# Optimization experiments

Hardware: AMD Instinct MI355X
Metric: run time of the kernel (lower is better)

Reference implementation:

```python
import jax, jax.numpy as jnp
import numpy as np

F, H1, H2, K, L = 16, 64, 64, 8, 8          # n_features, hidden sizes, num_bins, num_layers
NBP = 3 * K + 1                              # num_bijector_params per feature
RMIN, RMAX = -10.0, 10.0
MIN_BIN, MIN_SLOPE = 1e-4, 1e-4              # distrax RationalQuadraticSpline defaults


def setup_inputs() -> dict:
    key = jax.random.key(0)
    ks = jax.random.split(key, 11)
    B = 131072
    return {
        "x": jax.random.normal(ks[0], (B, F), jnp.float32),
        "W0": jax.random.normal(ks[1], (L, F, F), jnp.float32) * 0.1,
        "b0": jax.random.normal(ks[2], (L, F), jnp.float32) * 0.01,
        "W1": jax.random.normal(ks[3], (L, F, H1), jnp.float32) * 0.1,
        "b1": jax.random.normal(ks[4], (L, H1), jnp.float32) * 0.01,
        "W2": jax.random.normal(ks[5], (L, H1, H2), jnp.float32) * 0.1,
        "b2": jax.random.normal(ks[6], (L, H2), jnp.float32) * 0.01,
        "Wout": jax.random.normal(ks[7], (L, H2, F * NBP), jnp.float32) * 0.05,
        "bout": jax.random.normal(ks[8], (L, F * NBP), jnp.float32) * 0.01,
        # scalar-affine coupling params; scale kept positive (init is ones in the module)
        "scale": jnp.exp(0.05 * jax.random.normal(ks[9], (L, F), jnp.float32)),
        "shift": jax.random.normal(ks[10], (L, F), jnp.float32) * 0.1,
    }


def _rq_spline_fwd(params, x):
    """distrax.RationalQuadraticSpline forward_and_log_det (elementwise).
    params: (B, F, 3K+1), x: (B, F) -> (y, log_det) each (B, F)."""
    uw, uh, ud = params[..., :K], params[..., K:2 * K], params[..., 2 * K:]
    total = RMAX - RMIN
    w = jax.nn.softmax(uw, axis=-1) * (total - K * MIN_BIN) + MIN_BIN   # bin widths
    h = jax.nn.softmax(uh, axis=-1) * (total - K * MIN_BIN) + MIN_BIN   # bin heights
    offset = float(np.log(np.expm1(1.0 - MIN_SLOPE)))                   # softplus(0+offset)=1
    d = jax.nn.softplus(ud + offset) + MIN_SLOPE                        # knot slopes (B,F,K+1)
    zeros = jnp.zeros(w.shape[:-1] + (1,), w.dtype)
    xpos = RMIN + jnp.concatenate([zeros, jnp.cumsum(w, -1)], -1)       # knot x (B,F,K+1)
    ypos = RMIN + jnp.concatenate([zeros, jnp.cumsum(h, -1)], -1)       # knot y (B,F,K+1)
    # per-element bin search
    idx = jnp.clip(jnp.sum((x[..., None] >= xpos).astype(jnp.int32), -1) - 1, 0, K - 1)
    take = lambda a: jnp.take_along_axis(a, idx[..., None], axis=-1)[..., 0]
    xk, xk1 = take(xpos[..., :-1]), take(xpos[..., 1:])
    yk, yk1 = take(ypos[..., :-1]), take(ypos[..., 1:])
    dk, dk1 = take(d[..., :-1]), take(d[..., 1:])
    bw = xk1 - xk
    bh = yk1 - yk
    s = bh / bw                                                          # bin slope
    z = jnp.clip((x - xk) / bw, 0.0, 1.0)
    z1m = 1.0 - z
    den = s + (dk1 + dk - 2.0 * s) * z * z1m
    y = yk + bh * (s * z * z + dk * z * z1m) / den
    num_ld = dk1 * z * z + 2.0 * s * z * z1m + dk * z1m * z1m
    ld = 2.0 * jnp.log(s) + jnp.log(num_ld) - 2.0 * jnp.log(den)
    outside = (x <= RMIN) | (x >= RMAX)                                  # identity outside range
    return jnp.where(outside, x, y), jnp.where(outside, 0.0, ld)


def reference(x, W0, b0, W1, b1, W2, b2, Wout, bout, scale, shift):
    """log_prob of Transformed(base, Inverse(Chain(layers))) == base.log_prob(Chain.fwd(x)) + fwd logdet."""
    B = x.shape[0]
    feat = jnp.arange(F)
    z = x
    logdet = jnp.zeros((B,), x.dtype)
    # distrax.Chain applies the last-appended layer first -> iterate layers in reverse;
    # within layer i: spline coupling (appended second) then scalar-affine coupling.
    for i in reversed(range(L)):
        mask = ((feat + i) % 2).astype(bool)        # True = pass-through / conditioner input
        mz = jnp.where(mask, z, 0.0)
        hid = jnp.tanh(mz @ W0[i] + b0[i])
        hid = jnp.tanh(hid @ W1[i] + b1[i])
        hid = hid @ W2[i] + b2[i]                   # last MLP layer is linear
        p = (hid @ Wout[i] + bout[i]).reshape(B, F, NBP)
        y, ld = _rq_spline_fwd(p, z)
        z = jnp.where(mask, z, y)
        logdet = logdet + jnp.sum(jnp.where(mask, 0.0, ld), axis=-1)
        # scalar affine coupling with all-False mask: transforms every feature
        z = z * scale[i] + shift[i]
        logdet = logdet + jnp.sum(jnp.log(jnp.abs(scale[i])))
    base_lp = -0.5 * jnp.sum(z * z, axis=-1) - 0.5 * F * float(np.log(2.0 * np.pi))
    return base_lp + logdet
```

## Files before the change

### kernel.cpp

```cpp
#include <hip/hip_runtime.h>
#include <math.h>

typedef _Float16 f16;
typedef _Float16 half4 __attribute__((ext_vector_type(4)));
typedef _Float16 half8 __attribute__((ext_vector_type(8)));
typedef float f32x4  __attribute__((ext_vector_type(4)));
typedef float f32x16 __attribute__((ext_vector_type(16)));

#define DEV __device__ __forceinline__

#define W1F_OFF 0
#define W2F_OFF 16384
#define WOF_OFF 81920
#define B1T_OFF 344064
#define B2T_OFF 346112
#define SUMLOG_OFF 352256
#define W0F_OFF 352320
#define B0T_OFF 361088
#define BOT_OFF 363136

#define H0_OFF    0
#define H0_STRIDE 48
#define H_OFF     3072
#define H_STRIDE  152
#define P_OFF     0
#define P_STRIDE  112
#define ARENA     12800
#define LDS_BYTES (4 * ARENA)

DEV float frcp(float x){ return __builtin_amdgcn_rcpf(x); }

#if __has_builtin(__builtin_amdgcn_exp2f)
DEV float fexp2(float x){ return __builtin_amdgcn_exp2f(x); }
#else
DEV float fexp2(float x){ return exp2f(x); }
#endif
#if __has_builtin(__builtin_amdgcn_logf)
DEV float flog2(float x){ return __builtin_amdgcn_logf(x); }
#else
DEV float flog2(float x){ return log2f(x); }
#endif

#define LN2F    0.69314718056f
#define LOG2EF  1.4426950409f
#define TWOLOG2EF 2.8853900818f

DEV float ftanh2(float x){
  float e = fexp2(x);
  float r = frcp(e + 1.f);
  return fmaf(-2.f, r, 1.f);
}

DEV void rq_spline(const float p[25], float xv, float &y_out, float &ld_out)
{
  float ew[8]; float sw = 0.f;
#pragma unroll
  for (int k = 0; k < 8; ++k){ ew[k] = fexp2(p[k]); sw += ew[k]; }
  float rw = frcp(sw) * 19.9992f;

  float xpos[9];
  xpos[0] = -10.f;
#pragma unroll
  for (int k = 0; k < 8; ++k) xpos[k + 1] = xpos[k] + fmaf(ew[k], rw, 1e-4f);

  bool b[8];
  int idx = 0;
#pragma unroll
  for (int j = 1; j < 8; ++j){ b[j] = (xv >= xpos[j]); idx += b[j] ? 1 : 0; }

  float xk = xpos[0], ewk = ew[0];
#pragma unroll
  for (int j = 1; j < 8; ++j){
    xk  = b[j] ? xpos[j] : xk;
    ewk = b[j] ? ew[j]   : ewk;
  }
  float bw = fmaf(ewk, rw, 1e-4f);

  float eh[8]; float shs = 0.f;
#pragma unroll
  for (int k = 0; k < 8; ++k){ eh[k] = fexp2(p[8 + k]); shs += eh[k]; }
  float rh = frcp(shs) * 19.9992f;

  float S = 0.f, ehk = eh[0];
#pragma unroll
  for (int k = 1; k < 8; ++k){
    S   += b[k] ? eh[k - 1] : 0.f;
    ehk  = b[k] ? eh[k]     : ehk;
  }
  float yk = fmaf(S, rh, fmaf((float)idx, 1e-4f, -10.f));
  float bh = fmaf(ehk, rh, 1e-4f);

  float vA = p[16], vB = p[17];
#pragma unroll
  for (int j = 1; j < 8; ++j){
    vA = b[j] ? p[16 + j] : vA;
    vB = b[j] ? p[17 + j] : vB;
  }
  float tA = fmaxf(vA, 0.f) + flog2(1.f + fexp2(-fabsf(vA)));
  float dk  = fmaf(LN2F, tA, 1e-4f);
  float tB = fmaxf(vB, 0.f) + flog2(1.f + fexp2(-fabsf(vB)));
  float dk1 = fmaf(LN2F, tB, 1e-4f);

  float rbw = frcp(bw);
  float s   = bh * rbw;
  float zf  = fminf(fmaxf((xv - xk) * rbw, 0.f), 1.f);
  float z1  = 1.f - zf;
  float zz  = zf * zf, z01 = zf * z1;
  float den = s + (dk1 + dk - 2.f * s) * z01;
  float rden = frcp(den);
  float yv  = yk + bh * (s * zz + dk * z01) * rden;
  float num = dk1 * zz + 2.f * s * z01 + dk * z1 * z1;
  float ldv2 = flog2(s * s * num * rden * rden);

  bool outside = (xv <= -10.f) || (xv >= 10.f);
  y_out  = outside ? xv : yv;
  ld_out = outside ? 0.f : ldv2;
}

extern "C" __global__ void __launch_bounds__(256)
prep_kernel(const float* __restrict__ W0, const float* __restrict__ b0,
            const float* __restrict__ W1, const float* __restrict__ b1,
            const float* __restrict__ W2, const float* __restrict__ b2,
            const float* __restrict__ Wo, const float* __restrict__ bout,
            const float* __restrict__ scale, char* __restrict__ ws)
{
  int tid = blockIdx.x * 256 + threadIdx.x;
  if (tid < 1024){
    int fi = tid >> 6, lane = tid & 63;
    int l = fi >> 1, nt = fi & 1;
    int n = nt * 32 + (lane & 31), khi = lane >> 5;
    half8 h;
#pragma unroll
    for (int j = 0; j < 8; ++j){ int k = khi * 8 + j; h[j] = (f16)(W1[l * 1024 + k * 64 + n] * TWOLOG2EF); }
    *(half8*)(ws + W1F_OFF + fi * 1024 + lane * 16) = h;
  } else if (tid < 5120){
    int idx = tid - 1024;
    int fi = idx >> 6, lane = idx & 63;
    int l = fi >> 3, kt = (fi >> 1) & 3, nt = fi & 1;
    int n = nt * 32 + (lane & 31), khi = lane >> 5;
    half8 h;
#pragma unroll
    for (int j = 0; j < 8; ++j){ int k = kt * 16 + khi * 8 + j; h[j] = (f16)W2[l * 4096 + k * 64 + n]; }
    *(half8*)(ws + W2F_OFF + fi * 1024 + lane * 16) = h;
  } else if (tid < 21504){
    int idx = tid - 5120;
    int fi = idx >> 6, lane = idx & 63;
    int l = fi >> 5, u = (fi >> 2) & 7, kt = fi & 3;
    int f = (l & 1) + 2 * u;
    int c = lane & 31, khi = lane >> 5;
    half8 h;
#pragma unroll
    for (int j = 0; j < 8; ++j){
      int k = kt * 16 + khi * 8 + j;
      float v = (c < 25) ? Wo[l * 25600 + k * 400 + f * 25 + c] * LOG2EF : 0.f;
      h[j] = (f16)v;
    }
    *(half8*)(ws + WOF_OFF + fi * 1024 + lane * 16) = h;
  } else if (tid < 22016){
    int idx = tid - 21504;
    int l = idx >> 6, nt = (idx >> 5) & 1, kh = (idx >> 4) & 1, i = idx & 15;
    int r = (i & 3) + 8 * (i >> 2) + 4 * kh;
    ((float*)(ws + B1T_OFF))[idx] = b1[l * 64 + nt * 32 + r] * TWOLOG2EF;
  } else if (tid < 22528){
    int idx = tid - 22016;
    int l = idx >> 6, nt = (idx >> 5) & 1, kh = (idx >> 4) & 1, i = idx & 15;
    int r = (i & 3) + 8 * (i >> 2) + 4 * kh;
    ((float*)(ws + B2T_OFF))[idx] = b2[l * 64 + nt * 32 + r];
  } else if (tid == 23552){
    float acc = 0.f;
    for (int i = 0; i < 128; ++i) acc += logf(fabsf(scale[i]));
    *(float*)(ws + SUMLOG_OFF) = acc;
  } else if (tid > 23552 && tid < 24065){
    int idx = tid - 23553;
    int l = idx >> 6, lane = idx & 63;
    int n = lane & 31, kh5 = lane >> 5;
    half8 h;
#pragma unroll
    for (int j = 0; j < 8; ++j){
      int k = kh5 * 8 + j;
      float v = 0.f;
      if (n < 16 && (((k + l) & 1) == 1))
        v = W0[l * 256 + k * 16 + n] * TWOLOG2EF;
      h[j] = (f16)v;
    }
    *(half8*)(ws + W0F_OFF + idx * 16) = h;
  } else if (tid >= 24065 && tid < 24321){
    int idx = tid - 24065;
    int l = idx >> 5, kh = (idx >> 4) & 1, i = idx & 15;
    int r = (i & 3) + 8 * (i >> 2) + 4 * kh;
    float v = (r < 16) ? b0[l * 16 + r] * TWOLOG2EF : 0.f;
    ((float*)(ws + B0T_OFF))[idx] = v;
  } else if (tid >= 26241 && tid < 28289){
    int idx = tid - 26241;
    int l = idx >> 8, u = (idx >> 5) & 7, kh = (idx >> 4) & 1, i = idx & 15;
    int f = (l & 1) + 2 * u;
    int r = (i & 3) + 8 * (i >> 2) + 4 * kh;
    float v = 0.f;
    if (r < 25){
      v = bout[l * 400 + f * 25 + r];
      if (r >= 16) v += 0.54116666f;
      v *= LOG2EF;
    }
    ((float*)(ws + BOT_OFF))[idx] = v;
  }
}

DEV void load_botv(const char* __restrict__ ws, int l, int u, int khi,
                   float (&botv)[16])
{
  const f32x4* bp = (const f32x4*)(ws + BOT_OFF) + ((l * 8 + u) * 2 + khi) * 4;
  f32x4 q0 = bp[0], q1 = bp[1], q2 = bp[2], q3 = bp[3];
#pragma unroll
  for (int i = 0; i < 4; ++i){
    botv[i] = q0[i]; botv[4 + i] = q1[i]; botv[8 + i] = q2[i]; botv[12 + i] = q3[i];
  }
}

DEV half8 ld_h8_pair(const char* p)
{
  half4 lo = *(const half4*)(p);
  half4 hi = *(const half4*)(p + 8);
  half8 r;
#pragma unroll
  for (int i = 0; i < 4; ++i){ r[i] = lo[i]; r[4 + i] = hi[i]; }
  return r;
}

DEV void wout_feature(const half8 (&a2)[2][4], const half8 (&bfn)[4],
                      const float (&botv)[16], char* ldsw, int ln31, int khi)
{
  f32x16 dp[2];
#pragma unroll
  for (int mt = 0; mt < 2; ++mt)
#pragma unroll
    for (int i = 0; i < 16; ++i) dp[mt][i] = botv[i];
#pragma unroll
  for (int kt = 0; kt < 4; ++kt)
#pragma unroll
    for (int mt = 0; mt < 2; ++mt)
      dp[mt] = __builtin_amdgcn_mfma_f32_32x32x16_f16(bfn[kt], a2[mt][kt], dp[mt], 0, 0, 0);
#pragma unroll
  for (int mt = 0; mt < 2; ++mt){
    int s = mt * 32 + ln31;
    char* base = ldsw + P_OFF + s * P_STRIDE + khi * 16;
    f32x4 c0, c1, c2;
#pragma unroll
    for (int i = 0; i < 4; ++i){
      c0[i] = dp[mt][i];
      c1[i] = dp[mt][4 + i];
      c2[i] = dp[mt][8 + i];
    }
    *(f32x4*)(base)      = c0;
    *(f32x4*)(base + 32) = c1;
    *(f32x4*)(base + 64) = c2;
    if (khi == 0)
      *(float*)(base + 96) = dp[mt][12];
  }
}

template<int PAR>
DEV void layer_mfma(int l,
                    const float* __restrict__ scv, const float* __restrict__ shv,
                    const char* __restrict__ ws, char* ldsw,
                    float (&z)[16], float &logdet,
                    int lane, int ln31, int khi)
{
  const half8* W1F = (const half8*)(ws + W1F_OFF);
  const half8* W2F = (const half8*)(ws + W2F_OFF);
  half8 w0f = *(const half8*)(ws + W0F_OFF + (l * 64 + lane) * 16);
  half8 w1f[2];
#pragma unroll
  for (int nt = 0; nt < 2; ++nt) w1f[nt] = W1F[(l * 2 + nt) * 64 + lane];
  half8 w2f[8];
#pragma unroll
  for (int kt = 0; kt < 4; ++kt)
#pragma unroll
    for (int nt = 0; nt < 2; ++nt)
      w2f[kt * 2 + nt] = W2F[((l * 4 + kt) * 2 + nt) * 64 + lane];

  {
    half8 zlo, zhi;
#pragma unroll
    for (int j = 0; j < 8; ++j){ zlo[j] = (f16)z[j]; zhi[j] = (f16)z[8 + j]; }
    *(half8*)(ldsw + H0_OFF + lane * H0_STRIDE)      = zlo;
    *(half8*)(ldsw + H0_OFF + lane * H0_STRIDE + 16) = zhi;
  }
  f32x16 d0t[2];
  {
    const f32x4* bp = (const f32x4*)(ws + B0T_OFF) + (l * 2 + khi) * 4;
    f32x4 q0 = bp[0], q1 = bp[1], q2 = bp[2], q3 = bp[3];
#pragma unroll
    for (int mt = 0; mt < 2; ++mt)
#pragma unroll
      for (int i = 0; i < 4; ++i){
        d0t[mt][i] = q0[i]; d0t[mt][4 + i] = q1[i];
        d0t[mt][8 + i] = q2[i]; d0t[mt][12 + i] = q3[i];
      }
  }
  {
    half8 zf[2];
#pragma unroll
    for (int mt = 0; mt < 2; ++mt)
      zf[mt] = *(const half8*)(ldsw + H0_OFF + (mt * 32 + ln31) * H0_STRIDE + khi * 16);
#pragma unroll
    for (int mt = 0; mt < 2; ++mt)
      d0t[mt] = __builtin_amdgcn_mfma_f32_32x32x16_f16(w0f, zf[mt], d0t[mt], 0, 0, 0);
  }
#pragma unroll
  for (int mt = 0; mt < 2; ++mt){
    int s = mt * 32 + ln31;
#pragma unroll
    for (int g = 0; g < 2; ++g){
      half4 h4;
#pragma unroll
      for (int j = 0; j < 4; ++j) h4[j] = (f16)ftanh2(d0t[mt][g * 4 + j]);
      *(half4*)(ldsw + H0_OFF + s * H0_STRIDE + g * 16 + khi * 8) = h4;
    }
  }

  half8 a0[2];
#pragma unroll
  for (int mt = 0; mt < 2; ++mt)
    a0[mt] = *(const half8*)(ldsw + H0_OFF + (mt * 32 + ln31) * H0_STRIDE + khi * 16);
  f32x16 d1t[2][2];
  {
    const f32x4* B1T = (const f32x4*)(ws + B1T_OFF);
#pragma unroll
    for (int nt = 0; nt < 2; ++nt){
      const f32x4* bp = B1T + ((l * 2 + nt) * 2 + khi) * 4;
      f32x4 q0 = bp[0], q1 = bp[1], q2 = bp[2], q3 = bp[3];
#pragma unroll
      for (int mt = 0; mt < 2; ++mt)
#pragma unroll
        for (int i = 0; i < 4; ++i){
          d1t[nt][mt][i] = q0[i]; d1t[nt][mt][4 + i] = q1[i];
          d1t[nt][mt][8 + i] = q2[i]; d1t[nt][mt][12 + i] = q3[i];
        }
    }
  }
#pragma unroll
  for (int nt = 0; nt < 2; ++nt)
#pragma unroll
    for (int mt = 0; mt < 2; ++mt)
      d1t[nt][mt] = __builtin_amdgcn_mfma_f32_32x32x16_f16(w1f[nt], a0[mt], d1t[nt][mt], 0, 0, 0);
#pragma unroll
  for (int nt = 0; nt < 2; ++nt)
#pragma unroll
    for (int mt = 0; mt < 2; ++mt){
      int s = mt * 32 + ln31;
#pragma unroll
      for (int g = 0; g < 4; ++g){
        half4 h4;
#pragma unroll
        for (int j = 0; j < 4; ++j) h4[j] = (f16)ftanh2(d1t[nt][mt][g * 4 + j]);
        *(half4*)(ldsw + H_OFF + s * H_STRIDE + nt * 64 + g * 16 + khi * 8) = h4;
      }
    }

  half8 a1[2][4];
#pragma unroll
  for (int mt = 0; mt < 2; ++mt)
#pragma unroll
    for (int kt = 0; kt < 4; ++kt)
      a1[mt][kt] = ld_h8_pair(ldsw + H_OFF + (mt * 32 + ln31) * H_STRIDE + kt * 32 + khi * 16);
  f32x16 d2t[2][2];
  {
    const f32x4* B2T = (const f32x4*)(ws + B2T_OFF);
#pragma unroll
    for (int nt = 0; nt < 2; ++nt){
      const f32x4* bp = B2T + ((l * 2 + nt) * 2 + khi) * 4;
      f32x4 q0 = bp[0], q1 = bp[1], q2 = bp[2], q3 = bp[3];
#pragma unroll
      for (int mt = 0; mt < 2; ++mt)
#pragma unroll
        for (int i = 0; i < 4; ++i){
          d2t[nt][mt][i] = q0[i]; d2t[nt][mt][4 + i] = q1[i];
          d2t[nt][mt][8 + i] = q2[i]; d2t[nt][mt][12 + i] = q3[i];
        }
    }
  }
#pragma unroll
  for (int kt = 0; kt < 4; ++kt)
#pragma unroll
    for (int nt = 0; nt < 2; ++nt)
#pragma unroll
      for (int mt = 0; mt < 2; ++mt)
        d2t[nt][mt] = __builtin_amdgcn_mfma_f32_32x32x16_f16(w2f[kt * 2 + nt], a1[mt][kt], d2t[nt][mt], 0, 0, 0);

  const half8* WOF = (const half8*)(ws + WOF_OFF);
  half8 bfn[4];
#pragma unroll
  for (int kt = 0; kt < 4; ++kt) bfn[kt] = WOF[((l * 8 + 0) * 4 + kt) * 64 + lane];
  float botv[16];
  load_botv(ws, l, 0, khi, botv);

#pragma unroll
  for (int nt = 0; nt < 2; ++nt)
#pragma unroll
    for (int mt = 0; mt < 2; ++mt){
      int s = mt * 32 + ln31;
#pragma unroll
      for (int g = 0; g < 4; ++g){
        half4 h4;
#pragma unroll
        for (int j = 0; j < 4; ++j) h4[j] = (f16)d2t[nt][mt][g * 4 + j];
        *(half4*)(ldsw + H_OFF + s * H_STRIDE + nt * 64 + g * 16 + khi * 8) = h4;
      }
    }

  half8 a2[2][4];
#pragma unroll
  for (int mt = 0; mt < 2; ++mt)
#pragma unroll
    for (int kt = 0; kt < 4; ++kt)
      a2[mt][kt] = ld_h8_pair(ldsw + H_OFF + (mt * 32 + ln31) * H_STRIDE + kt * 32 + khi * 16);

  wout_feature(a2, bfn, botv, ldsw, ln31, khi);
#pragma unroll
  for (int kt = 0; kt < 4; ++kt) bfn[kt] = WOF[((l * 8 + 1) * 4 + kt) * 64 + lane];
  load_botv(ws, l, 1, khi, botv);

#pragma unroll 2
  for (int u = 0; u < 8; ++u){
    float p[25];
    {
      const char* pb = ldsw + P_OFF + lane * P_STRIDE;
#pragma unroll
      for (int q = 0; q < 6; ++q){
        f32x4 v = *(const f32x4*)(pb + q * 16);
#pragma unroll
        for (int i = 0; i < 4; ++i) p[q * 4 + i] = v[i];
      }
      p[24] = *(const float*)(pb + 96);
    }

    if (u < 7){
      wout_feature(a2, bfn, botv, ldsw, ln31, khi);
      if (u < 6){
#pragma unroll
        for (int kt = 0; kt < 4; ++kt) bfn[kt] = WOF[((l * 8 + u + 2) * 4 + kt) * 64 + lane];
        load_botv(ws, l, u + 2, khi, botv);
      }
    }

    const int f = PAR + 2 * u;
    float y, ld;
    rq_spline(p, z[f], y, ld);
    z[f] = y;
    logdet += ld;
  }

  const float* scp = scv + l * 16;
  const float* shp = shv + l * 16;
#pragma unroll
  for (int j = 0; j < 16; ++j)
    z[j] = fmaf(z[j], scp[j], shp[j]);
}

extern "C" __global__ void __launch_bounds__(256, 2)
flow_kernel(const float* __restrict__ x,
            const float* __restrict__ scv, const float* __restrict__ shv,
            const char* __restrict__ ws, float* __restrict__ out, int B)
{
  extern __shared__ char lds[];
  const int t    = threadIdx.x;
  const int lane = t & 63;
  const int wv   = t >> 6;
  const int ln31 = lane & 31;
  const int khi  = lane >> 5;
  char* ldsw = lds + wv * ARENA;
  const int g = blockIdx.x * 256 + t;

  float z[16];
  const float4* xv = reinterpret_cast<const float4*>(x + (size_t)g * 16);
  float4 a0 = xv[0], a1 = xv[1], a2 = xv[2], a3 = xv[3];
  z[0]=a0.x; z[1]=a0.y; z[2]=a0.z; z[3]=a0.w;
  z[4]=a1.x; z[5]=a1.y; z[6]=a1.z; z[7]=a1.w;
  z[8]=a2.x; z[9]=a2.y; z[10]=a2.z; z[11]=a2.w;
  z[12]=a3.x; z[13]=a3.y; z[14]=a3.z; z[15]=a3.w;

  float logdet = 0.f;
  for (int l = 7; l >= 0; --l){
    if (l & 1) layer_mfma<1>(l, scv, shv, ws, ldsw, z, logdet, lane, ln31, khi);
    else       layer_mfma<0>(l, scv, shv, ws, ldsw, z, logdet, lane, ln31, khi);
  }

  float sumlog = *(const float*)(ws + SUMLOG_OFF);
  float ss = 0.f;
#pragma unroll
  for (int j = 0; j < 16; ++j) ss = fmaf(z[j], z[j], ss);
  out[g] = fmaf(LN2F, logdet, -0.5f * ss - 14.7030165f + sumlog);
}

extern "C" void kernel_launch(void* const* d_in, const int* in_sizes, int n_in,
                              void* d_out, int out_size, void* d_ws, size_t ws_size,
                              hipStream_t stream)
{
  const float* x    = (const float*)d_in[0];
  const float* W0   = (const float*)d_in[1];
  const float* b0   = (const float*)d_in[2];
  const float* W1   = (const float*)d_in[3];
  const float* b1   = (const float*)d_in[4];
  const float* W2   = (const float*)d_in[5];
  const float* b2   = (const float*)d_in[6];
  const float* Wout = (const float*)d_in[7];
  const float* bout = (const float*)d_in[8];
  const float* scale= (const float*)d_in[9];
  const float* shift= (const float*)d_in[10];

  int B = in_sizes[0] / 16;

  hipLaunchKernelGGL(prep_kernel, dim3(111), dim3(256), 0, stream,
                     W0, b0, W1, b1, W2, b2, Wout, bout, scale, (char*)d_ws);

  hipLaunchKernelGGL(flow_kernel, dim3(B / 256), dim3(256), LDS_BYTES, stream,
                     x, scale, shift,
                     (const char*)d_ws, (float*)d_out, B);
}
```

Before: 181.8 us.

## Split each sample across two lanes so each wave handles 32 samples

Each wave now processes 32 samples instead of 64. The two half-waves (khi) each own one sample of a 32-wide MFMA tile and evaluate splines for different features in parallel, then exchange results with a cross-lane shuffle. Wout products are computed two features at a time into two LDS slots. The grid doubles, per-wave LDS shrinks, and the redundant z/logdet per lane pair lowers register pressure per MFMA tile. In exchange, x loads and the MLP work are duplicated across half-waves, and the number of waves doubles.

Measured after the change: 196.1 us. +7.9%, slower.

```diff
diff --git a/kernel.cpp b/kernel.cpp
--- a/kernel.cpp
+++ b/kernel.cpp
@@ -21,11 +21,12 @@
 
 #define H0_OFF    0
 #define H0_STRIDE 48
-#define H_OFF     3072
+#define H_OFF     1536
 #define H_STRIDE  152
 #define P_OFF     0
 #define P_STRIDE  112
-#define ARENA     12800
+#define P_SLOT    3584
+#define ARENA     7168
 #define LDS_BYTES (4 * ARENA)
 
 DEV float frcp(float x){ return __builtin_amdgcn_rcpf(x); }
@@ -226,35 +227,35 @@
   return r;
 }
 
-DEV void wout_feature(const half8 (&a2)[2][4], const half8 (&bfn)[4],
-                      const float (&botv)[16], char* ldsw, int ln31, int khi)
-{
-  f32x16 dp[2];
-#pragma unroll
-  for (int mt = 0; mt < 2; ++mt)
-#pragma unroll
-    for (int i = 0; i < 16; ++i) dp[mt][i] = botv[i];
-#pragma unroll
-  for (int kt = 0; kt < 4; ++kt)
-#pragma unroll
-    for (int mt = 0; mt < 2; ++mt)
-      dp[mt] = __builtin_amdgcn_mfma_f32_32x32x16_f16(bfn[kt], a2[mt][kt], dp[mt], 0, 0, 0);
-#pragma unroll
-  for (int mt = 0; mt < 2; ++mt){
-    int s = mt * 32 + ln31;
-    char* base = ldsw + P_OFF + s * P_STRIDE + khi * 16;
+DEV void wout_pair(const half8 (&a2)[4],
+                   const half8 (&bfnA)[4], const half8 (&bfnB)[4],
+                   const float (&botvA)[16], const float (&botvB)[16],
+                   char* ldsw, int ln31, int khi)
+{
+  f32x16 dpA, dpB;
+#pragma unroll
+  for (int i = 0; i < 16; ++i){ dpA[i] = botvA[i]; dpB[i] = botvB[i]; }
+#pragma unroll
+  for (int kt = 0; kt < 4; ++kt){
+    dpA = __builtin_amdgcn_mfma_f32_32x32x16_f16(bfnA[kt], a2[kt], dpA, 0, 0, 0);
+    dpB = __builtin_amdgcn_mfma_f32_32x32x16_f16(bfnB[kt], a2[kt], dpB, 0, 0, 0);
+  }
+#pragma unroll
+  for (int sl = 0; sl < 2; ++sl){
+    const f32x16 &dp = sl ? dpB : dpA;
+    char* base = ldsw + P_OFF + sl * P_SLOT + ln31 * P_STRIDE + khi * 16;
     f32x4 c0, c1, c2;
 #pragma unroll
     for (int i = 0; i < 4; ++i){
-      c0[i] = dp[mt][i];
-      c1[i] = dp[mt][4 + i];
-      c2[i] = dp[mt][8 + i];
+      c0[i] = dp[i];
+      c1[i] = dp[4 + i];
+      c2[i] = dp[8 + i];
     }
     *(f32x4*)(base)      = c0;
     *(f32x4*)(base + 32) = c1;
     *(f32x4*)(base + 64) = c2;
     if (khi == 0)
-      *(float*)(base + 96) = dp[mt][12];
+      *(float*)(base + 96) = dp[12];
   }
 }
 
@@ -278,51 +279,34 @@
     for (int nt = 0; nt < 2; ++nt)
       w2f[kt * 2 + nt] = W2F[((l * 4 + kt) * 2 + nt) * 64 + lane];
 
+  half8 zf;
   {
     half8 zlo, zhi;
 #pragma unroll
     for (int j = 0; j < 8; ++j){ zlo[j] = (f16)z[j]; zhi[j] = (f16)z[8 + j]; }
-    *(half8*)(ldsw + H0_OFF + lane * H0_STRIDE)      = zlo;
-    *(half8*)(ldsw + H0_OFF + lane * H0_STRIDE + 16) = zhi;
-  }
-  f32x16 d0t[2];
+#pragma unroll
+    for (int j = 0; j < 8; ++j) zf[j] = khi ? zhi[j] : zlo[j];
+  }
+  f32x16 d0t;
   {
     const f32x4* bp = (const f32x4*)(ws + B0T_OFF) + (l * 2 + khi) * 4;
     f32x4 q0 = bp[0], q1 = bp[1], q2 = bp[2], q3 = bp[3];
 #pragma unroll
-    for (int mt = 0; mt < 2; ++mt)
-#pragma unroll
-      for (int i = 0; i < 4; ++i){
-        d0t[mt][i] = q0[i]; d0t[mt][4 + i] = q1[i];
-        d0t[mt][8 + i] = q2[i]; d0t[mt][12 + i] = q3[i];
-      }
-  }
-  {
-    half8 zf[2];
-#pragma unroll
-    for (int mt = 0; mt < 2; ++mt)
-      zf[mt] = *(const half8*)(ldsw + H0_OFF + (mt * 32 + ln31) * H0_STRIDE + khi * 16);
-#pragma unroll
-    for (int mt = 0; mt < 2; ++mt)
-      d0t[mt] = __builtin_amdgcn_mfma_f32_32x32x16_f16(w0f, zf[mt], d0t[mt], 0, 0, 0);
-  }
-#pragma unroll
-  for (int mt = 0; mt < 2; ++mt){
-    int s = mt * 32 + ln31;
-#pragma unroll
-    for (int g = 0; g < 2; ++g){
-      half4 h4;
-#pragma unroll
-      for (int j = 0; j < 4; ++j) h4[j] = (f16)ftanh2(d0t[mt][g * 4 + j]);
-      *(half4*)(ldsw + H0_OFF + s * H0_STRIDE + g * 16 + khi * 8) = h4;
-    }
-  }
-
-  half8 a0[2];
-#pragma unroll
-  for (int mt = 0; mt < 2; ++mt)
-    a0[mt] = *(const half8*)(ldsw + H0_OFF + (mt * 32 + ln31) * H0_STRIDE + khi * 16);
-  f32x16 d1t[2][2];
+    for (int i = 0; i < 4; ++i){
+      d0t[i] = q0[i]; d0t[4 + i] = q1[i]; d0t[8 + i] = q2[i]; d0t[12 + i] = q3[i];
+    }
+  }
+  d0t = __builtin_amdgcn_mfma_f32_32x32x16_f16(w0f, zf, d0t, 0, 0, 0);
+#pragma unroll
+  for (int g = 0; g < 2; ++g){
+    half4 h4;
+#pragma unroll
+    for (int j = 0; j < 4; ++j) h4[j] = (f16)ftanh2(d0t[g * 4 + j]);
+    *(half4*)(ldsw + H0_OFF + ln31 * H0_STRIDE + g * 16 + khi * 8) = h4;
+  }
+
+  half8 a0 = *(const half8*)(ldsw + H0_OFF + ln31 * H0_STRIDE + khi * 16);
+  f32x16 d1t[2];
   {
     const f32x4* B1T = (const f32x4*)(ws + B1T_OFF);
 #pragma unroll
@@ -330,40 +314,30 @@
       const f32x4* bp = B1T + ((l * 2 + nt) * 2 + khi) * 4;
       f32x4 q0 = bp[0], q1 = bp[1], q2 = bp[2], q3 = bp[3];
 #pragma unroll
-      for (int mt = 0; mt < 2; ++mt)
-#pragma unroll
-        for (int i = 0; i < 4; ++i){
-          d1t[nt][mt][i] = q0[i]; d1t[nt][mt][4 + i] = q1[i];
-          d1t[nt][mt][8 + i] = q2[i]; d1t[nt][mt][12 + i] = q3[i];
-        }
+      for (int i = 0; i < 4; ++i){
+        d1t[nt][i] = q0[i]; d1t[nt][4 + i] = q1[i];
+        d1t[nt][8 + i] = q2[i]; d1t[nt][12 + i] = q3[i];
+      }
     }
   }
 #pragma unroll
   for (int nt = 0; nt < 2; ++nt)
-#pragma unroll
-    for (int mt = 0; mt < 2; ++mt)
-      d1t[nt][mt] = __builtin_amdgcn_mfma_f32_32x32x16_f16(w1f[nt], a0[mt], d1t[nt][mt], 0, 0, 0);
+    d1t[nt] = __builtin_amdgcn_mfma_f32_32x32x16_f16(w1f[nt], a0, d1t[nt], 0, 0, 0);
 #pragma unroll
   for (int nt = 0; nt < 2; ++nt)
 #pragma unroll
-    for (int mt = 0; mt < 2; ++mt){
-      int s = mt * 32 + ln31;
-#pragma unroll
-      for (int g = 0; g < 4; ++g){
-        half4 h4;
-#pragma unroll
-        for (int j = 0; j < 4; ++j) h4[j] = (f16)ftanh2(d1t[nt][mt][g * 4 + j]);
-        *(half4*)(ldsw + H_OFF + s * H_STRIDE + nt * 64 + g * 16 + khi * 8) = h4;
-      }
-    }
-
-  half8 a1[2][4];
-#pragma unroll
-  for (int mt = 0; mt < 2; ++mt)
-#pragma unroll
-    for (int kt = 0; kt < 4; ++kt)
-      a1[mt][kt] = ld_h8_pair(ldsw + H_OFF + (mt * 32 + ln31) * H_STRIDE + kt * 32 + khi * 16);
-  f32x16 d2t[2][2];
+    for (int g = 0; g < 4; ++g){
+      half4 h4;
+#pragma unroll
+      for (int j = 0; j < 4; ++j) h4[j] = (f16)ftanh2(d1t[nt][g * 4 + j]);
+      *(half4*)(ldsw + H_OFF + ln31 * H_STRIDE + nt * 64 + g * 16 + khi * 8) = h4;
+    }
+
+  half8 a1[4];
+#pragma unroll
+  for (int kt = 0; kt < 4; ++kt)
+    a1[kt] = ld_h8_pair(ldsw + H_OFF + ln31 * H_STRIDE + kt * 32 + khi * 16);
+  f32x16 d2t[2];
   {
     const f32x4* B2T = (const f32x4*)(ws + B2T_OFF);
 #pragma unroll
@@ -371,82 +345,88 @@
       const f32x4* bp = B2T + ((l * 2 + nt) * 2 + khi) * 4;
       f32x4 q0 = bp[0], q1 = bp[1], q2 = bp[2], q3 = bp[3];
 #pragma unroll
-      for (int mt = 0; mt < 2; ++mt)
-#pragma unroll
-        for (int i = 0; i < 4; ++i){
-          d2t[nt][mt][i] = q0[i]; d2t[nt][mt][4 + i] = q1[i];
-          d2t[nt][mt][8 + i] = q2[i]; d2t[nt][mt][12 + i] = q3[i];
-        }
+      for (int i = 0; i < 4; ++i){
+        d2t[nt][i] = q0[i]; d2t[nt][4 + i] = q1[i];
+        d2t[nt][8 + i] = q2[i]; d2t[nt][12 + i] = q3[i];
+      }
     }
   }
 #pragma unroll
   for (int kt = 0; kt < 4; ++kt)
 #pragma unroll
     for (int nt = 0; nt < 2; ++nt)
-#pragma unroll
-      for (int mt = 0; mt < 2; ++mt)
-        d2t[nt][mt] = __builtin_amdgcn_mfma_f32_32x32x16_f16(w2f[kt * 2 + nt], a1[mt][kt], d2t[nt][mt], 0, 0, 0);
+      d2t[nt] = __builtin_amdgcn_mfma_f32_32x32x16_f16(w2f[kt * 2 + nt], a1[kt], d2t[nt], 0, 0, 0);
 
   const half8* WOF = (const half8*)(ws + WOF_OFF);
-  half8 bfn[4];
-#pragma unroll
-  for (int kt = 0; kt < 4; ++kt) bfn[kt] = WOF[((l * 8 + 0) * 4 + kt) * 64 + lane];
-  float botv[16];
-  load_botv(ws, l, 0, khi, botv);
+  half8 bfnA[4], bfnB[4];
+#pragma unroll
+  for (int kt = 0; kt < 4; ++kt){
+    bfnA[kt] = WOF[((l * 8 + 0) * 4 + kt) * 64 + lane];
+    bfnB[kt] = WOF[((l * 8 + 1) * 4 + kt) * 64 + lane];
+  }
+  float botvA[16], botvB[16];
+  load_botv(ws, l, 0, khi, botvA);
+  load_botv(ws, l, 1, khi, botvB);
 
 #pragma unroll
   for (int nt = 0; nt < 2; ++nt)
 #pragma unroll
-    for (int mt = 0; mt < 2; ++mt){
-      int s = mt * 32 + ln31;
-#pragma unroll
-      for (int g = 0; g < 4; ++g){
-        half4 h4;
-#pragma unroll
-        for (int j = 0; j < 4; ++j) h4[j] = (f16)d2t[nt][mt][g * 4 + j];
-        *(half4*)(ldsw + H_OFF + s * H_STRIDE + nt * 64 + g * 16 + khi * 8) = h4;
-      }
-    }
-
-  half8 a2[2][4];
-#pragma unroll
-  for (int mt = 0; mt < 2; ++mt)
-#pragma unroll
-    for (int kt = 0; kt < 4; ++kt)
-      a2[mt][kt] = ld_h8_pair(ldsw + H_OFF + (mt * 32 + ln31) * H_STRIDE + kt * 32 + khi * 16);
-
-  wout_feature(a2, bfn, botv, ldsw, ln31, khi);
-#pragma unroll
-  for (int kt = 0; kt < 4; ++kt) bfn[kt] = WOF[((l * 8 + 1) * 4 + kt) * 64 + lane];
-  load_botv(ws, l, 1, khi, botv);
-
-#pragma unroll 2
-  for (int u = 0; u < 8; ++u){
+    for (int g = 0; g < 4; ++g){
+      half4 h4;
+#pragma unroll
+      for (int j = 0; j < 4; ++j) h4[j] = (f16)d2t[nt][g * 4 + j];
+      *(half4*)(ldsw + H_OFF + ln31 * H_STRIDE + nt * 64 + g * 16 + khi * 8) = h4;
+    }
+
+  half8 a2[4];
+#pragma unroll
+  for (int kt = 0; kt < 4; ++kt)
+    a2[kt] = ld_h8_pair(ldsw + H_OFF + ln31 * H_STRIDE + kt * 32 + khi * 16);
+
+  wout_pair(a2, bfnA, bfnB, botvA, botvB, ldsw, ln31, khi);
+#pragma unroll
+  for (int kt = 0; kt < 4; ++kt){
+    bfnA[kt] = WOF[((l * 8 + 2) * 4 + kt) * 64 + lane];
+    bfnB[kt] = WOF[((l * 8 + 3) * 4 + kt) * 64 + lane];
+  }
+  load_botv(ws, l, 2, khi, botvA);
+  load_botv(ws, l, 3, khi, botvB);
+
+#pragma unroll
+  for (int v = 0; v < 4; ++v){
     float p[25];
     {
-      const char* pb = ldsw + P_OFF + lane * P_STRIDE;
+      const char* pb = ldsw + P_OFF + khi * P_SLOT + ln31 * P_STRIDE;
 #pragma unroll
       for (int q = 0; q < 6; ++q){
-        f32x4 v = *(const f32x4*)(pb + q * 16);
-#pragma unroll
-        for (int i = 0; i < 4; ++i) p[q * 4 + i] = v[i];
+        f32x4 vq = *(const f32x4*)(pb + q * 16);
+#pragma unroll
+        for (int i = 0; i < 4; ++i) p[q * 4 + i] = vq[i];
       }
       p[24] = *(const float*)(pb + 96);
     }
 
-    if (u < 7){
-      wout_feature(a2, bfn, botv, ldsw, ln31, khi);
-      if (u < 6){
-#pragma unroll
-        for (int kt = 0; kt < 4; ++kt) bfn[kt] = WOF[((l * 8 + u + 2) * 4 + kt) * 64 + lane];
-        load_botv(ws, l, u + 2, khi, botv);
+    if (v < 3){
+      wout_pair(a2, bfnA, bfnB, botvA, botvB, ldsw, ln31, khi);
+      if (v < 2){
+#pragma unroll
+        for (int kt = 0; kt < 4; ++kt){
+          bfnA[kt] = WOF[((l * 8 + 2 * v + 4) * 4 + kt) * 64 + lane];
+          bfnB[kt] = WOF[((l * 8 + 2 * v + 5) * 4 + kt) * 64 + lane];
+        }
+        load_botv(ws, l, 2 * v + 4, khi, botvA);
+        load_botv(ws, l, 2 * v + 5, khi, botvB);
       }
     }
 
-    const int f = PAR + 2 * u;
+    const int fA = PAR + 4 * v;
+    const int fB = fA + 2;
+    float xv = khi ? z[fB] : z[fA];
     float y, ld;
-    rq_spline(p, z[f], y, ld);
-    z[f] = y;
+    rq_spline(p, xv, y, ld);
+    float yx = __shfl_xor(y, 32, 64);
+    z[fA] = khi ? yx : y;
+    z[fB] = khi ? y  : yx;
     logdet += ld;
   }
 
@@ -469,11 +449,11 @@
   const int ln31 = lane & 31;
   const int khi  = lane >> 5;
   char* ldsw = lds + wv * ARENA;
-  const int g = blockIdx.x * 256 + t;
+  const int g = blockIdx.x * 128 + wv * 32 + ln31;
 
   float z[16];
-  const float4* xv = reinterpret_cast<const float4*>(x + (size_t)g * 16);
-  float4 a0 = xv[0], a1 = xv[1], a2 = xv[2], a3 = xv[3];
+  const float4* xv4 = reinterpret_cast<const float4*>(x + (size_t)g * 16);
+  float4 a0 = xv4[0], a1 = xv4[1], a2 = xv4[2], a3 = xv4[3];
   z[0]=a0.x; z[1]=a0.y; z[2]=a0.z; z[3]=a0.w;
   z[4]=a1.x; z[5]=a1.y; z[6]=a1.z; z[7]=a1.w;
   z[8]=a2.x; z[9]=a2.y; z[10]=a2.z; z[11]=a2.w;
@@ -485,11 +465,14 @@
     else       layer_mfma<0>(l, scv, shv, ws, ldsw, z, logdet, lane, ln31, khi);
   }
 
+  logdet += __shfl_xor(logdet, 32, 64);
+
   float sumlog = *(const float*)(ws + SUMLOG_OFF);
   float ss = 0.f;
 #pragma unroll
   for (int j = 0; j < 16; ++j) ss = fmaf(z[j], z[j], ss);
-  out[g] = fmaf(LN2F, logdet, -0.5f * ss - 14.7030165f + sumlog);
+  if (khi == 0)
+    out[g] = fmaf(LN2F, logdet, -0.5f * ss - 14.7030165f + sumlog);
 }
 
 extern "C" void kernel_launch(void* const* d_in, const int* in_sizes, int n_in,
@@ -513,7 +496,7 @@
   hipLaunchKernelGGL(prep_kernel, dim3(111), dim3(256), 0, stream,
                      W0, b0, W1, b1, W2, b2, Wout, bout, scale, (char*)d_ws);
 
-  hipLaunchKernelGGL(flow_kernel, dim3(B / 256), dim3(256), LDS_BYTES, stream,
+  hipLaunchKernelGGL(flow_kernel, dim3(B / 128), dim3(256), LDS_BYTES, stream,
                      x, scale, shift,
                      (const char*)d_ws, (float*)d_out, B);
 }
```
